# Optimization experiments

Measured on AMD Instinct MI355X. Metric: run time of the kernel, lower is better.

The kernel has to match this reference:

```python
import jax, jax.numpy as jnp
import numpy as np

EPS = 1e-5

def setup_inputs() -> dict:
    key = jax.random.key(0)
    ks = jax.random.split(key, 5)
    B, L, D = 8, 2048, 1024
    scale = 0.02
    return {
        "x": jax.random.normal(ks[0], (B, L, D), dtype=jnp.float32),
        "Wk": jax.random.normal(ks[1], (D, D), dtype=jnp.float32) * scale,
        "Wkg": jax.random.normal(ks[2], (D, D), dtype=jnp.float32) * scale,
        "bkg": jnp.zeros((D,), dtype=jnp.float32),
        "Wout": jax.random.normal(ks[3], (D, D), dtype=jnp.float32) * scale,
        "num_heads": 16,
    }

def reference(x, Wk, Wkg, bkg, Wout, num_heads):
    B, L, D = x.shape
    n = num_heads
    d = D // n  # per-head dim
    k = x @ Wk.T                                   # [B, L, D]
    g = jax.nn.sigmoid(x @ Wkg.T + bkg)            # [B, L, D]
    # [B, L, n, d] -> scan over L
    k = k.reshape(B, L, n, d).transpose(1, 0, 2, 3)  # [L, B, n, d]
    g = g.reshape(B, L, n, d).transpose(1, 0, 2, 3)
    inv_sqrt_d = 1.0 / np.sqrt(d)

    def step(h, xs):
        x_t, g_t = xs
        rms = jnp.sqrt(jnp.sum(h * h, axis=-1, keepdims=True)) * inv_sqrt_d
        h_hat = h / (rms + EPS)
        h_new = h_hat * g_t + x_t
        return h_new, h_new

    h0 = jnp.zeros((B, n, d), dtype=x.dtype)
    _, o = jax.lax.scan(step, h0, (k, g))          # [L, B, n, d]
    o = o.transpose(1, 0, 2, 3).reshape(B, L, D)   # [B, L, D]
    return o @ Wout.T
```

## Files before the change

### kernel.cpp

```cpp
#include <hip/hip_runtime.h>
#include <hip/hip_bf16.h>
#include <math.h>

#define BATCH 8
#define SEQL  2048
#define DIM   1024
#define MROWS (BATCH * SEQL)

typedef _Float16 f16;
typedef _Float16 f16x8 __attribute__((ext_vector_type(8)));
typedef _Float16 f16x4 __attribute__((ext_vector_type(4)));
typedef _Float16 f16x2 __attribute__((ext_vector_type(2)));
typedef float f32x4 __attribute__((ext_vector_type(4)));

typedef const __attribute__((address_space(1))) void* gp_t;
typedef __attribute__((address_space(3))) void* lp_t;
#define GLL(src, dst) __builtin_amdgcn_global_load_lds((gp_t)(src), (lp_t)(dst), 16, 0, 0)

__global__ __launch_bounds__(256) void cvt_all(const float* __restrict__ x,
                                               const float* __restrict__ Wk,
                                               const float* __restrict__ Wkg,
                                               const float* __restrict__ Wout,
                                               f16* __restrict__ xh,
                                               f16* __restrict__ Wcat,
                                               f16* __restrict__ Wouth)
{
    int i = blockIdx.x * 256 + threadIdx.x;
    const float* src; f16* dst;
    if (i < 2097152)      { src = x;    dst = xh;             }
    else if (i < 2228224) { src = Wk;   dst = Wcat;           i -= 2097152; }
    else if (i < 2359296) { src = Wkg;  dst = Wcat + 1048576; i -= 2228224; }
    else                  { src = Wout; dst = Wouth;          i -= 2359296; }
    const float4* p = (const float4*)src + (size_t)i * 2;
    const float4 a = p[0], b = p[1];
    f16x8 v;
    v[0] = (f16)a.x; v[1] = (f16)a.y; v[2] = (f16)a.z; v[3] = (f16)a.w;
    v[4] = (f16)b.x; v[5] = (f16)b.y; v[6] = (f16)b.z; v[7] = (f16)b.w;
    *(f16x8*)(dst + (size_t)i * 8) = v;
}

template<int MODE>
__global__ __launch_bounds__(512, 2) void gemm8(const f16* __restrict__ A,
                                                const f16* __restrict__ Bw,
                                                const float* __restrict__ bias,
                                                void* __restrict__ C0,
                                                void* __restrict__ C1)
{
    constexpr int K   = 1024;
    constexpr int NTI = MODE ? 8 : 4;
    constexpr int NKT = 16;
    __shared__ f16 ldsA[256 * 64];
    __shared__ f16 ldsB[256 * 64];

    const int tid = threadIdx.x;
    const int w = tid >> 6, l = tid & 63;
    const int wm = w >> 2, wn = w & 3;
    const int lrow = l & 15;
    const int l7 = l & 7, lk = l >> 4;

    const int cpx = gridDim.x >> 3;
    const int lt  = (blockIdx.x & 7) * cpx + (blockIdx.x >> 3);
    const int bm  = (lt / NTI) * 256;
    const int bn  = (lt % NTI) * 256;

    const int srl   = tid >> 3;
    const int sg    = tid & 7;
    const int scolx = (sg ^ (srl & 7)) * 8;
    const int aR0 = (srl < 32) ? srl : (96 + srl);

    const int g0 = ((lk) ^ l7) * 8;
    const int g1 = ((4 + lk) ^ l7) * 8;

#define STAGE_AQ(tt, p)                                                                  \
    do {                                                                                 \
        const int _R = 32 * (p) + aR0;                                                   \
        GLL(A + (size_t)(bm + _R) * K + (tt) * 64 + scolx, ldsA + _R * 64 + sg * 8);     \
    } while (0)

#define STAGE_BH(tt, h)                                                                  \
    do {                                                                                 \
        const int _r0 = (h) * 128 + srl;                                                 \
        GLL(Bw + (size_t)(bn + _r0) * K + (tt) * 64 + scolx, ldsB + _r0 * 64 + sg * 8);  \
        const int _r1 = _r0 + 64;                                                        \
        GLL(Bw + (size_t)(bn + _r1) * K + (tt) * 64 + scolx, ldsB + _r1 * 64 + sg * 8);  \
    } while (0)

    f32x4 acc[8][4];
    #pragma unroll
    for (int mi = 0; mi < 8; ++mi)
        #pragma unroll
        for (int ni = 0; ni < 4; ++ni) acc[mi][ni] = (f32x4){0.f, 0.f, 0.f, 0.f};

    f16x8 bf[4][2];

#define PHASE(p, VK, STG)                                                                \
    do {                                                                                 \
        asm volatile("s_waitcnt vmcnt(" #VK ")" ::: "memory");                           \
        __builtin_amdgcn_s_barrier();                                                    \
        const int _ar = (wm * 128 + 32 * (p) + lrow) * 64;                               \
        f16x8 a00 = *(const f16x8*)(ldsA + _ar + g0);                                    \
        f16x8 a01 = *(const f16x8*)(ldsA + _ar + g1);                                    \
        f16x8 a10 = *(const f16x8*)(ldsA + _ar + 1024 + g0);                             \
        f16x8 a11 = *(const f16x8*)(ldsA + _ar + 1024 + g1);                             \
        if ((p) == 0) {                                                                  \
            _Pragma("unroll")                                                            \
            for (int ni = 0; ni < 4; ++ni) {                                             \
                const int _br = (wn * 64 + ni * 16 + lrow) * 64;                         \
                bf[ni][0] = *(const f16x8*)(ldsB + _br + g0);                            \
                bf[ni][1] = *(const f16x8*)(ldsB + _br + g1);                            \
            }                                                                            \
        }                                                                                \
        STG;                                                                             \
        asm volatile("s_waitcnt lgkmcnt(0)" ::: "memory");                               \
        __builtin_amdgcn_sched_barrier(0);                                               \
        __builtin_amdgcn_s_setprio(1);                                                   \
        _Pragma("unroll")                                                                \
        for (int ni = 0; ni < 4; ++ni) {                                                 \
            acc[2*(p)][ni]   = __builtin_amdgcn_mfma_f32_16x16x32_f16(a00, bf[ni][0], acc[2*(p)][ni], 0, 0, 0);   \
            acc[2*(p)][ni]   = __builtin_amdgcn_mfma_f32_16x16x32_f16(a01, bf[ni][1], acc[2*(p)][ni], 0, 0, 0);   \
            acc[2*(p)+1][ni] = __builtin_amdgcn_mfma_f32_16x16x32_f16(a10, bf[ni][0], acc[2*(p)+1][ni], 0, 0, 0); \
            acc[2*(p)+1][ni] = __builtin_amdgcn_mfma_f32_16x16x32_f16(a11, bf[ni][1], acc[2*(p)+1][ni], 0, 0, 0); \
        }                                                                                \
        __builtin_amdgcn_s_setprio(0);                                                   \
    } while (0)

    STAGE_BH(0, 0); STAGE_AQ(0, 0);
    STAGE_BH(0, 1); STAGE_AQ(0, 1);
    STAGE_AQ(0, 2);

    for (int t = 0; t < NKT - 1; ++t) {
        PHASE(0, 2, { STAGE_AQ(t, 3); });
        PHASE(1, 2, { STAGE_BH(t + 1, 0); STAGE_AQ(t + 1, 0); });
        PHASE(2, 4, { STAGE_BH(t + 1, 1); STAGE_AQ(t + 1, 1); });
        PHASE(3, 6, { STAGE_AQ(t + 1, 2); });
    }
    PHASE(0, 2, { STAGE_AQ(NKT - 1, 3); });
    PHASE(1, 2, {});
    PHASE(2, 1, {});
    PHASE(3, 0, {});
#undef PHASE
#undef STAGE_AQ
#undef STAGE_BH

    const int orow = (l >> 4) * 4;
    const int ocol = l & 15;
    #pragma unroll
    for (int mi = 0; mi < 8; ++mi) {
        #pragma unroll
        for (int ni = 0; ni < 4; ++ni) {
            const int col  = bn + wn * 64 + ni * 16 + ocol;
            const int row0 = bm + wm * 128 + mi * 16 + orow;
            #pragma unroll
            for (int r = 0; r < 4; ++r) {
                float v = acc[mi][ni][r];
                if (MODE == 0) {
                    ((float*)C0)[(size_t)(row0 + r) * DIM + col] = v;
                } else {
                    if (col < DIM) {
                        ((f16*)C0)[(size_t)(row0 + r) * DIM + col] = (f16)v;
                    } else {
                        v += bias[col - DIM];
                        v = 1.f / (1.f + __expf(-v));
                        ((f16*)C1)[(size_t)(row0 + r) * DIM + (col - DIM)] = (f16)v;
                    }
                }
            }
        }
    }
}

template<int CTRL>
__device__ __forceinline__ float dpp_add_f(float s) {
    int t = __builtin_amdgcn_update_dpp(0, __float_as_int(s), CTRL, 0xF, 0xF, true);
    return s + __int_as_float(t);
}

__device__ __forceinline__ float sumsq4(f16x2 a, f16x2 b) {
    return __builtin_amdgcn_fdot2(a, a, __builtin_amdgcn_fdot2(b, b, 0.f, false), false);
}

#define PF 16
#define CHK 128
#define WARM 128

__global__ __launch_bounds__(64) void scan_kernel(const f16* __restrict__ Kv,
                                                  const f16* __restrict__ Gv,
                                                  f16* __restrict__ Ov)
{
    const int w = blockIdx.x & 31;
    const int c = blockIdx.x >> 5;
    const int l = threadIdx.x;

    const int t0   = (c == 0) ? 0 : (c * CHK - WARM);
    const int warm = c * CHK - t0;

    const size_t base = (size_t)(w >> 2) * (SEQL * DIM) + (size_t)((w & 3) * 256 + l * 4);
    size_t off = base + (size_t)t0 * DIM;

    f16x2 h01 = (f16x2){(f16)0.f, (f16)0.f};
    f16x2 h23 = (f16x2){(f16)0.f, (f16)0.f};

    f16x4 kb[PF], gb[PF];
    #pragma unroll
    for (int u = 0; u < PF; ++u) {
        kb[u] = *(const f16x4*)(Kv + off + (size_t)u * DIM);
        gb[u] = *(const f16x4*)(Gv + off + (size_t)u * DIM);
    }

    #define SCAN_STEP(kc, gc, DO_ST)                                                   \
        do {                                                                           \
            const f16x2 k01 = __builtin_shufflevector((kc), (kc), 0, 1);               \
            const f16x2 k23 = __builtin_shufflevector((kc), (kc), 2, 3);               \
            const f16x2 g01 = __builtin_shufflevector((gc), (gc), 0, 1);               \
            const f16x2 g23 = __builtin_shufflevector((gc), (gc), 2, 3);               \
            const f16x2 u01 = h01 * g01;                                               \
            const f16x2 u23 = h23 * g23;                                               \
            float s = sumsq4(h01, h23);                                                \
            s = dpp_add_f<0xB1>(s);                                                    \
            s = dpp_add_f<0x4E>(s);                                                    \
            s = dpp_add_f<0x141>(s);                                                   \
            s = dpp_add_f<0x140>(s);                                                   \
            const float inv = __builtin_amdgcn_rsqf(fmaf(s, 0.015625f, 1e-8f));        \
            const f16 ih = (f16)inv;                                                   \
            const f16x2 iv = (f16x2){ih, ih};                                          \
            h01 = u01 * iv + k01;                                                      \
            h23 = u23 * iv + k23;                                                      \
            if (DO_ST) {                                                               \
                f16x4 o;                                                               \
                o[0] = h01[0]; o[1] = h01[1]; o[2] = h23[0]; o[3] = h23[1];            \
                *(f16x4*)(Ov + off) = o;                                               \
            }                                                                          \
            off += DIM;                                                                \
        } while (0)

    for (int tb = 0; tb < warm; tb += PF) {
        #pragma unroll
        for (int u = 0; u < PF; ++u) {
            const f16x4 kc = kb[u], gc = gb[u];
            const size_t poff = off + (size_t)PF * DIM;
            kb[u] = *(const f16x4*)(Kv + poff);
            gb[u] = *(const f16x4*)(Gv + poff);
            SCAN_STEP(kc, gc, 0);
        }
    }
    for (int tb = 0; tb < CHK - PF; tb += PF) {
        #pragma unroll
        for (int u = 0; u < PF; ++u) {
            const f16x4 kc = kb[u], gc = gb[u];
            const size_t poff = off + (size_t)PF * DIM;
            kb[u] = *(const f16x4*)(Kv + poff);
            gb[u] = *(const f16x4*)(Gv + poff);
            SCAN_STEP(kc, gc, 1);
        }
    }
    #pragma unroll
    for (int u = 0; u < PF; ++u) {
        const f16x4 kc = kb[u], gc = gb[u];
        SCAN_STEP(kc, gc, 1);
    }
    #undef SCAN_STEP
}

extern "C" void kernel_launch(void* const* d_in, const int* in_sizes, int n_in,
                              void* d_out, int out_size, void* d_ws, size_t ws_size,
                              hipStream_t stream) {
    const float* x    = (const float*)d_in[0];
    const float* Wk   = (const float*)d_in[1];
    const float* Wkg  = (const float*)d_in[2];
    const float* bkg  = (const float*)d_in[3];
    const float* Wout = (const float*)d_in[4];
    float* out = (float*)d_out;

    f16* xh    = (f16*)d_ws;
    f16* Kh    = xh    + (size_t)MROWS * DIM;
    f16* Gh    = Kh    + (size_t)MROWS * DIM;
    f16* Wcat  = Gh    + (size_t)MROWS * DIM;
    f16* Wouth = Wcat  + (size_t)2 * DIM * DIM;

    cvt_all<<<dim3(9728), dim3(256), 0, stream>>>(x, Wk, Wkg, Wout, xh, Wcat, Wouth);

    gemm8<1><<<dim3(512), dim3(512), 0, stream>>>(xh, Wcat, bkg, Kh, Gh);
    scan_kernel<<<dim3(512), dim3(64), 0, stream>>>(Kh, Gh, xh);
    gemm8<0><<<dim3(256), dim3(512), 0, stream>>>(xh, Wouth, nullptr, out, nullptr);
}
```

Measured before the change: 186.0 us.

## Double GEMM K-tile depth to 128 to halve barrier phases

Widens the per-iteration K slice in the f16 MFMA GEMM from 64 to 128, doubling the LDS tiles and halving the number of K iterations. Staging loads, swizzled fragment reads, B-fragment registers and vmcnt wait counts are all reworked to match. The goal is to run more MFMAs per barrier and waitcnt, cutting synchronisation overhead. The cost is double the LDS (128 KB per block), which may drop occupancy from the 2 blocks per CU requested by launch bounds, plus extra fragment registers.

After: 264.3 us. +42.1%, slower.

```diff
diff --git a/kernel.cpp b/kernel.cpp
--- a/kernel.cpp
+++ b/kernel.cpp
@@ -48,9 +48,9 @@
 {
     constexpr int K   = 1024;
     constexpr int NTI = MODE ? 8 : 4;
-    constexpr int NKT = 16;
-    __shared__ f16 ldsA[256 * 64];
-    __shared__ f16 ldsB[256 * 64];
+    constexpr int NKT = 8;
+    __shared__ f16 ldsA[256 * 128];
+    __shared__ f16 ldsB[256 * 128];
 
     const int tid = threadIdx.x;
     const int w = tid >> 6, l = tid & 63;
@@ -63,26 +63,26 @@
     const int bm  = (lt / NTI) * 256;
     const int bn  = (lt % NTI) * 256;
 
-    const int srl   = tid >> 3;
-    const int sg    = tid & 7;
+    const int srl   = tid >> 4;
+    const int sg    = tid & 15;
     const int scolx = (sg ^ (srl & 7)) * 8;
-    const int aR0 = (srl < 32) ? srl : (96 + srl);
-
-    const int g0 = ((lk) ^ l7) * 8;
-    const int g1 = ((4 + lk) ^ l7) * 8;
 
 #define STAGE_AQ(tt, p)                                                                  \
     do {                                                                                 \
-        const int _R = 32 * (p) + aR0;                                                   \
-        GLL(A + (size_t)(bm + _R) * K + (tt) * 64 + scolx, ldsA + _R * 64 + sg * 8);     \
+        const int _R0 = 32 * (p) + srl;                                                  \
+        GLL(A + (size_t)(bm + _R0) * K + (tt) * 128 + scolx, ldsA + _R0 * 128 + sg * 8); \
+        const int _R1 = _R0 + 128;                                                       \
+        GLL(A + (size_t)(bm + _R1) * K + (tt) * 128 + scolx, ldsA + _R1 * 128 + sg * 8); \
     } while (0)
 
 #define STAGE_BH(tt, h)                                                                  \
     do {                                                                                 \
-        const int _r0 = (h) * 128 + srl;                                                 \
-        GLL(Bw + (size_t)(bn + _r0) * K + (tt) * 64 + scolx, ldsB + _r0 * 64 + sg * 8);  \
-        const int _r1 = _r0 + 64;                                                        \
-        GLL(Bw + (size_t)(bn + _r1) * K + (tt) * 64 + scolx, ldsB + _r1 * 64 + sg * 8);  \
+        _Pragma("unroll")                                                                \
+        for (int _rr = 0; _rr < 4; ++_rr) {                                              \
+            const int _R = (h) * 128 + _rr * 32 + srl;                                   \
+            GLL(Bw + (size_t)(bn + _R) * K + (tt) * 128 + scolx,                         \
+                ldsB + _R * 128 + sg * 8);                                               \
+        }                                                                                \
     } while (0)
 
     f32x4 acc[8][4];
@@ -91,23 +91,28 @@
         #pragma unroll
         for (int ni = 0; ni < 4; ++ni) acc[mi][ni] = (f32x4){0.f, 0.f, 0.f, 0.f};
 
-    f16x8 bf[4][2];
-
-#define PHASE(p, VK, STG)                                                                \
+    f16x8 bf[4][4];
+
+#define PHASE(p, VK, STG, LOAD_B)                                                        \
     do {                                                                                 \
         asm volatile("s_waitcnt vmcnt(" #VK ")" ::: "memory");                           \
         __builtin_amdgcn_s_barrier();                                                    \
-        const int _ar = (wm * 128 + 32 * (p) + lrow) * 64;                               \
-        f16x8 a00 = *(const f16x8*)(ldsA + _ar + g0);                                    \
-        f16x8 a01 = *(const f16x8*)(ldsA + _ar + g1);                                    \
-        f16x8 a10 = *(const f16x8*)(ldsA + _ar + 1024 + g0);                             \
-        f16x8 a11 = *(const f16x8*)(ldsA + _ar + 1024 + g1);                             \
-        if ((p) == 0) {                                                                  \
+        const int _r0 = (wm * 128 + 32 * (p) + lrow) * 128;                              \
+        const int _r1 = _r0 + 16 * 128;                                                  \
+        f16x8 a0[4], a1[4];                                                              \
+        _Pragma("unroll")                                                                \
+        for (int ks = 0; ks < 4; ++ks) {                                                 \
+            const int _gq = ((ks * 4 + lk) ^ l7) * 8;                                    \
+            a0[ks] = *(const f16x8*)(ldsA + _r0 + _gq);                                  \
+            a1[ks] = *(const f16x8*)(ldsA + _r1 + _gq);                                  \
+        }                                                                                \
+        if (LOAD_B) {                                                                    \
             _Pragma("unroll")                                                            \
             for (int ni = 0; ni < 4; ++ni) {                                             \
-                const int _br = (wn * 64 + ni * 16 + lrow) * 64;                         \
-                bf[ni][0] = *(const f16x8*)(ldsB + _br + g0);                            \
-                bf[ni][1] = *(const f16x8*)(ldsB + _br + g1);                            \
+                const int _br = (wn * 64 + ni * 16 + lrow) * 128;                        \
+                _Pragma("unroll")                                                        \
+                for (int ks = 0; ks < 4; ++ks)                                           \
+                    bf[ni][ks] = *(const f16x8*)(ldsB + _br + (((ks * 4 + lk) ^ l7) * 8)); \
             }                                                                            \
         }                                                                                \
         STG;                                                                             \
@@ -115,11 +120,12 @@
         __builtin_amdgcn_sched_barrier(0);                                               \
         __builtin_amdgcn_s_setprio(1);                                                   \
         _Pragma("unroll")                                                                \
-        for (int ni = 0; ni < 4; ++ni) {                                                 \
-            acc[2*(p)][ni]   = __builtin_amdgcn_mfma_f32_16x16x32_f16(a00, bf[ni][0], acc[2*(p)][ni], 0, 0, 0);   \
-            acc[2*(p)][ni]   = __builtin_amdgcn_mfma_f32_16x16x32_f16(a01, bf[ni][1], acc[2*(p)][ni], 0, 0, 0);   \
-            acc[2*(p)+1][ni] = __builtin_amdgcn_mfma_f32_16x16x32_f16(a10, bf[ni][0], acc[2*(p)+1][ni], 0, 0, 0); \
-            acc[2*(p)+1][ni] = __builtin_amdgcn_mfma_f32_16x16x32_f16(a11, bf[ni][1], acc[2*(p)+1][ni], 0, 0, 0); \
+        for (int ks = 0; ks < 4; ++ks) {                                                 \
+            _Pragma("unroll")                                                            \
+            for (int ni = 0; ni < 4; ++ni) {                                             \
+                acc[2*(p)][ni]   = __builtin_amdgcn_mfma_f32_16x16x32_f16(a0[ks], bf[ni][ks], acc[2*(p)][ni], 0, 0, 0);   \
+                acc[2*(p)+1][ni] = __builtin_amdgcn_mfma_f32_16x16x32_f16(a1[ks], bf[ni][ks], acc[2*(p)+1][ni], 0, 0, 0); \
+            }                                                                            \
         }                                                                                \
         __builtin_amdgcn_s_setprio(0);                                                   \
     } while (0)
@@ -129,15 +135,15 @@
     STAGE_AQ(0, 2);
 
     for (int t = 0; t < NKT - 1; ++t) {
-        PHASE(0, 2, { STAGE_AQ(t, 3); });
-        PHASE(1, 2, { STAGE_BH(t + 1, 0); STAGE_AQ(t + 1, 0); });
-        PHASE(2, 4, { STAGE_BH(t + 1, 1); STAGE_AQ(t + 1, 1); });
-        PHASE(3, 6, { STAGE_AQ(t + 1, 2); });
-    }
-    PHASE(0, 2, { STAGE_AQ(NKT - 1, 3); });
-    PHASE(1, 2, {});
-    PHASE(2, 1, {});
-    PHASE(3, 0, {});
+        PHASE(0, 4,  { STAGE_AQ(t, 3); }, 1);
+        PHASE(1, 4,  { STAGE_BH(t + 1, 0); STAGE_AQ(t + 1, 0); }, 0);
+        PHASE(2, 8,  { STAGE_BH(t + 1, 1); STAGE_AQ(t + 1, 1); }, 0);
+        PHASE(3, 12, { STAGE_AQ(t + 1, 2); }, 0);
+    }
+    PHASE(0, 4, { STAGE_AQ(NKT - 1, 3); }, 1);
+    PHASE(1, 4, {}, 0);
+    PHASE(2, 2, {}, 0);
+    PHASE(3, 0, {}, 0);
 #undef PHASE
 #undef STAGE_AQ
 #undef STAGE_BH
```
